# Kernel tuning notes

Hardware: AMD Instinct MI355X
Metric: run time of the kernel (lower is better)

The kernel has to match this reference:

```python
import jax, jax.numpy as jnp
import numpy as np

INF = 1e9  # large additive-mask constant (original code's INF)
D_KEY = 64


def setup_inputs() -> dict:
    key = jax.random.key(0)
    kq, kk, kv = jax.random.split(key, 3)
    B, S, D = 8, 2048, 64
    return {
        "query": jax.random.normal(kq, (B, S, D), dtype=jnp.float32),
        "key": jax.random.normal(kk, (B, S, D), dtype=jnp.float32),
        "value": jax.random.normal(kv, (B, S, D), dtype=jnp.float32),
    }


def reference(query, key, value):
    # scores: [B, Sq, Sk]
    scores = jnp.einsum("bqd,bkd->bqk", query, key)
    Sk = key.shape[1]
    # strict upper-triangular additive causal mask, subtracted BEFORE scaling
    tri = jnp.triu(jnp.ones((Sk, Sk), dtype=scores.dtype), k=1) * INF
    scores = scores - tri[None, :, :]
    scale = jnp.asarray(np.sqrt(D_KEY), dtype=scores.dtype)
    attn = jax.nn.softmax(scores / scale, axis=2)  # dropout ratio = 0.0
    return jnp.einsum("bqk,bkd->bqd", attn, value)
```

## Files before the change

### kernel.cpp

```cpp
#include <hip/hip_runtime.h>
#include <hip/hip_bf16.h>

typedef __attribute__((ext_vector_type(8))) short bf16x8;
typedef __attribute__((ext_vector_type(4))) float f32x4;
typedef __attribute__((ext_vector_type(4))) unsigned short us4;

#define BATCH 8
#define SEQ 2048
#define DIM 64
#define QB 64
#define NQT 32
#define NKT 32
#define TE 4096
#define CH 4
#define CPB 144
#define QSCALE (0.125f * 1.44269504088896f)
#define THR 8.0f

__device__ __forceinline__ unsigned short f2bf(float f) {
    return __builtin_bit_cast(unsigned short, __float2bfloat16(f));
}
__device__ __forceinline__ float bf2f(unsigned short u) {
    return __builtin_bit_cast(float, (unsigned)u << 16);
}

__device__ __forceinline__ int kswz(int row, int d) {
    return (row * DIM + d) ^ ((row & 7) << 3);
}
__device__ __forceinline__ int vswz(int d, int kv) {
    return (d * 64 + kv) ^ ((((d & 7) ^ ((d >> 2) & 7)) & 7) << 3);
}
__device__ __forceinline__ int pswz(int row, int kv) {
    return (row * 64 + kv) ^ ((row & 7) << 3);
}

#define GLOAD16(gsrc, ldst)                                                     \
    __builtin_amdgcn_global_load_lds(                                           \
        (const __attribute__((address_space(1))) void*)(gsrc),                  \
        (__attribute__((address_space(3))) void*)(ldst), 16, 0, 0)

__global__ __launch_bounds__(256) void prep_kernel(const float* __restrict__ K,
                                                   const float* __restrict__ V,
                                                   unsigned short* __restrict__ Kp,
                                                   unsigned short* __restrict__ Vp) {
    const int batch = blockIdx.x & 7;
    const int t = blockIdx.x >> 3;
    const int tile = batch * NKT + t;
    const int tid = threadIdx.x;
    const float* Kt = K + (size_t)tile * TE;
    const float* Vt = V + (size_t)tile * TE;
    unsigned short* Kd = Kp + (size_t)tile * TE;
    unsigned short* Vd = Vp + (size_t)tile * TE;
    #pragma unroll
    for (int i = 0; i < 4; ++i) {
        int idx = i * 256 + tid;
        int row = idx >> 4;
        int d0 = (idx & 15) << 2;
        f32x4 kf = *(const f32x4*)(Kt + row * DIM + d0);
        us4 kb = {f2bf(kf[0]), f2bf(kf[1]), f2bf(kf[2]), f2bf(kf[3])};
        *(us4*)(&Kd[kswz(row, d0)]) = kb;
    }
    const int dt4 = tid & 15, k4 = tid >> 4;
    f32x4 vf[4];
    #pragma unroll
    for (int rr = 0; rr < 4; ++rr)
        vf[rr] = *(const f32x4*)(Vt + (k4 * 4 + rr) * DIM + dt4 * 4);
    #pragma unroll
    for (int dd = 0; dd < 4; ++dd) {
        us4 vb = {f2bf(vf[0][dd]), f2bf(vf[1][dd]), f2bf(vf[2][dd]), f2bf(vf[3][dd])};
        *(us4*)(&Vd[vswz(dt4 * 4 + dd, k4 * 4)]) = vb;
    }
}

__global__ __launch_bounds__(256, 4) void fa_kernel(const float* __restrict__ Q,
                                                    const unsigned short* __restrict__ Kp,
                                                    const unsigned short* __restrict__ Vp,
                                                    unsigned short* __restrict__ PO,
                                                    float* __restrict__ PM,
                                                    float* __restrict__ PL,
                                                    float* __restrict__ O) {
    __shared__ unsigned short KL[2][4096];
    __shared__ unsigned short VL[2][4096];
    __shared__ unsigned short PB[4][1024];

    const int tid = threadIdx.x;
    const int w = tid >> 6, lane = tid & 63, g = lane >> 4, c = lane & 15;

    const int slot = blockIdx.x;
    const int batch = slot & 7;
    const int c0 = (CPB - 1) - (slot >> 3);
    int g2 = 0;
    #pragma unroll
    for (int gg = 1; gg < 8; ++gg) g2 = (c0 >= 2 * gg * (gg + 1)) ? gg : g2;
    const int nc = g2 + 1;
    const int x = c0 - 2 * g2 * nc;
    const int qrow = (x >= nc) + (x >= 2 * nc) + (x >= 3 * nc);
    const int sp = x - qrow * nc;
    const int qi = 4 * g2 + qrow;

    const int q0 = qi * QB;
    const int nt = qi + 1;
    const int t0 = sp * CH;
    const int t1 = (t0 + CH < nt) ? (t0 + CH) : nt;
    const int tiles = t1 - t0;
    const bool dchunk = (t1 == nt);

    const unsigned short* Kb = Kp + (size_t)batch * NKT * TE;
    const unsigned short* Vb = Vp + (size_t)batch * NKT * TE;

#define STAGE_TILE(tidx, buf)                                          \
    do {                                                               \
        const char* Ks_ = (const char*)(Kb + (size_t)(tidx) * TE);     \
        const char* Vs_ = (const char*)(Vb + (size_t)(tidx) * TE);     \
        char* kd_ = (char*)&KL[buf][0];                                \
        char* vd_ = (char*)&VL[buf][0];                                \
        _Pragma("unroll")                                              \
        for (int i_ = 0; i_ < 2; ++i_) {                               \
            int off_ = (w * 2 + i_) * 1024;                            \
            GLOAD16(Ks_ + off_ + lane * 16, kd_ + off_);               \
            GLOAD16(Vs_ + off_ + lane * 16, vd_ + off_);               \
        }                                                              \
    } while (0)

    STAGE_TILE(t0, 0);

    const float* Qrow = Q + (size_t)(batch * SEQ + q0 + w * 16 + c) * DIM;
    f32x4 qf0 = *(const f32x4*)(Qrow + g * 8);
    f32x4 qf1 = *(const f32x4*)(Qrow + g * 8 + 4);
    f32x4 qf2 = *(const f32x4*)(Qrow + 32 + g * 8);
    f32x4 qf3 = *(const f32x4*)(Qrow + 32 + g * 8 + 4);
    bf16x8 qa[2];
    #pragma unroll
    for (int j = 0; j < 4; ++j) {
        qa[0][j]     = (short)f2bf(qf0[j] * QSCALE);
        qa[0][j + 4] = (short)f2bf(qf1[j] * QSCALE);
        qa[1][j]     = (short)f2bf(qf2[j] * QSCALE);
        qa[1][j + 4] = (short)f2bf(qf3[j] * QSCALE);
    }

    float m[4], lsum[4];
    f32x4 o[4];
    #pragma unroll
    for (int r = 0; r < 4; ++r) { m[r] = -1e30f; lsum[r] = 0.f; }
    #pragma unroll
    for (int dt = 0; dt < 4; ++dt) o[dt] = f32x4{0.f, 0.f, 0.f, 0.f};

    __builtin_amdgcn_sched_barrier(0);
    asm volatile("s_waitcnt vmcnt(0)" ::: "memory");
    __builtin_amdgcn_s_barrier();
    __builtin_amdgcn_sched_barrier(0);

    for (int u = 0; u < tiles; ++u) {
        const int cb = u & 1;
        const bool last = (u == tiles - 1);

        if (!last) STAGE_TILE(t0 + u + 1, cb ^ 1);

        f32x4 s[4];
        #pragma unroll
        for (int n = 0; n < 4; ++n) s[n] = f32x4{0.f, 0.f, 0.f, 0.f};
        __builtin_amdgcn_s_setprio(1);
        #pragma unroll
        for (int n = 0; n < 4; ++n)
            #pragma unroll
            for (int f = 0; f < 2; ++f) {
                bf16x8 kb = *(bf16x8*)(&KL[cb][kswz(n * 16 + c, f * 32 + g * 8)]);
                s[n] = __builtin_amdgcn_mfma_f32_16x16x32_bf16(qa[f], kb, s[n], 0, 0, 0);
            }
        __builtin_amdgcn_s_setprio(0);

        if (dchunk && last) {
            const int dbase = (nt - 1) * 64;
            #pragma unroll
            for (int n = 0; n < 4; ++n) {
                int col = dbase + n * 16 + c;
                #pragma unroll
                for (int r = 0; r < 4; ++r)
                    if (col > q0 + w * 16 + g * 4 + r) s[n][r] = -1e30f;
            }
        }

        float pmx[4];
        #pragma unroll
        for (int r = 0; r < 4; ++r)
            pmx[r] = fmaxf(fmaxf(s[0][r], s[1][r]), fmaxf(s[2][r], s[3][r]));
        bool need = false;
        #pragma unroll
        for (int r = 0; r < 4; ++r) need |= (pmx[r] > m[r] + THR);
        if (__any(need)) {
            #pragma unroll
            for (int r = 0; r < 4; ++r) {
                float t2 = pmx[r];
                t2 = fmaxf(t2, __shfl_xor(t2, 1));
                t2 = fmaxf(t2, __shfl_xor(t2, 2));
                t2 = fmaxf(t2, __shfl_xor(t2, 4));
                t2 = fmaxf(t2, __shfl_xor(t2, 8));
                float mn = fmaxf(m[r], t2);
                float alpha = exp2f(m[r] - mn);
                m[r] = mn;
                lsum[r] *= alpha;
                #pragma unroll
                for (int dt = 0; dt < 4; ++dt) o[dt][r] *= alpha;
            }
        }
        #pragma unroll
        for (int n = 0; n < 4; ++n)
            #pragma unroll
            for (int r = 0; r < 4; ++r) {
                float pe = exp2f(s[n][r] - m[r]);
                s[n][r] = pe;
                lsum[r] += pe;
            }

        unsigned short* Pw = &PB[w][0];
        #pragma unroll
        for (int n = 0; n < 4; ++n)
            #pragma unroll
            for (int r = 0; r < 4; ++r)
                Pw[pswz(g * 4 + r, n * 16 + c)] = f2bf(s[n][r]);
        asm volatile("s_waitcnt lgkmcnt(0)" ::: "memory");
        __builtin_amdgcn_sched_barrier(0);

        __builtin_amdgcn_s_setprio(1);
        #pragma unroll
        for (int ks = 0; ks < 2; ++ks) {
            bf16x8 pa = *(bf16x8*)(&Pw[pswz(c, ks * 32 + g * 8)]);
            #pragma unroll
            for (int dt = 0; dt < 4; ++dt) {
                bf16x8 vb = *(bf16x8*)(&VL[cb][vswz(dt * 16 + c, ks * 32 + g * 8)]);
                o[dt] = __builtin_amdgcn_mfma_f32_16x16x32_bf16(pa, vb, o[dt], 0, 0, 0);
            }
        }
        __builtin_amdgcn_s_setprio(0);

        if (!last) {
            __builtin_amdgcn_sched_barrier(0);
            asm volatile("s_waitcnt vmcnt(0)" ::: "memory");
            __builtin_amdgcn_s_barrier();
            __builtin_amdgcn_sched_barrier(0);
        }
    }

    float l[4];
    #pragma unroll
    for (int r = 0; r < 4; ++r) {
        float ts = lsum[r];
        ts += __shfl_xor(ts, 1);
        ts += __shfl_xor(ts, 2);
        ts += __shfl_xor(ts, 4);
        ts += __shfl_xor(ts, 8);
        l[r] = ts;
    }

    if (nt <= CH) {
        #pragma unroll
        for (int r = 0; r < 4; ++r) {
            float inv = 1.f / l[r];
            float* Orow = O + (size_t)(batch * SEQ + q0 + w * 16 + g * 4 + r) * DIM;
            #pragma unroll
            for (int dt = 0; dt < 4; ++dt)
                Orow[dt * 16 + c] = o[dt][r] * inv;
        }
    } else {
        unsigned short* Pbase = PO + (size_t)slot * (QB * DIM);
        #pragma unroll
        for (int r = 0; r < 4; ++r) {
            int rowin = w * 16 + g * 4 + r;
            #pragma unroll
            for (int dt = 0; dt < 4; ++dt)
                Pbase[rowin * DIM + dt * 16 + c] = f2bf(o[dt][r]);
            if (c == 0) {
                PM[(size_t)slot * QB + rowin] = m[r];
                PL[(size_t)slot * QB + rowin] = l[r];
            }
        }
    }
#undef STAGE_TILE
}

__global__ __launch_bounds__(256) void combine_kernel(const unsigned short* __restrict__ PO,
                                                      const float* __restrict__ PM,
                                                      const float* __restrict__ PL,
                                                      float* __restrict__ O) {
    const int tid = threadIdx.x;
    const int ridx = blockIdx.x * 16 + (tid >> 4);
    const int d0 = (tid & 15) << 2;
    const int batch = ridx / 1792;
    const int rem = ridx - batch * 1792;
    const int qi = 4 + (rem >> 6);
    const int rowin = rem & 63;
    const int a = qi >> 2, b = qi & 3;
    const int nc = a + 1;
    const int pfx = (a + 1) * (2 * a + b);

    float mrun = -1e30f, ls = 0.f;
    f32x4 os = {0.f, 0.f, 0.f, 0.f};
    for (int sp = 0; sp < nc; ++sp) {
        int sl = ((CPB - 1 - (pfx + sp)) << 3) | batch;
        float mi = PM[(size_t)sl * QB + rowin];
        if (mi > mrun) {
            float sc = exp2f(mrun - mi);
            ls *= sc;
            os *= sc;
            mrun = mi;
        }
        float wgt = exp2f(mi - mrun);
        ls += PL[(size_t)sl * QB + rowin] * wgt;
        us4 po = *(const us4*)(PO + (size_t)sl * (QB * DIM) + rowin * DIM + d0);
        os[0] += bf2f(po[0]) * wgt;
        os[1] += bf2f(po[1]) * wgt;
        os[2] += bf2f(po[2]) * wgt;
        os[3] += bf2f(po[3]) * wgt;
    }
    const int grow = batch * SEQ + qi * 64 + rowin;
    float inv = 1.f / ls;
    f32x4 res = os * inv;
    *(f32x4*)(O + (size_t)grow * DIM + d0) = res;
}

extern "C" void kernel_launch(void* const* d_in, const int* in_sizes, int n_in,
                              void* d_out, int out_size, void* d_ws, size_t ws_size,
                              hipStream_t stream) {
    const float* Q = (const float*)d_in[0];
    const float* K = (const float*)d_in[1];
    const float* V = (const float*)d_in[2];
    float* O = (float*)d_out;
    (void)in_sizes; (void)n_in; (void)out_size; (void)ws_size;

    const size_t kvelems = (size_t)BATCH * SEQ * DIM;
    unsigned short* Kp = (unsigned short*)d_ws;
    unsigned short* Vp = Kp + kvelems;
    unsigned short* PO = Vp + kvelems;
    float* PM = (float*)(PO + (size_t)BATCH * CPB * QB * DIM);
    float* PL = PM + (size_t)BATCH * CPB * QB;

    prep_kernel<<<BATCH * NKT, 256, 0, stream>>>(K, V, Kp, Vp);
    fa_kernel<<<BATCH * CPB, 256, 0, stream>>>(Q, Kp, Vp, PO, PM, PL, O);
    combine_kernel<<<BATCH * 28 * 64 / 16, 256, 0, stream>>>(PO, PM, PL, O);
}
```

Baseline: 36.52 us.

## Compute transposed S so P stays in registers, dropping LDS round-trip for P

```diff
diff --git a/kernel.cpp b/kernel.cpp
--- a/kernel.cpp
+++ b/kernel.cpp
@@ -4,6 +4,7 @@
 typedef __attribute__((ext_vector_type(8))) short bf16x8;
 typedef __attribute__((ext_vector_type(4))) float f32x4;
 typedef __attribute__((ext_vector_type(4))) unsigned short us4;
+typedef __attribute__((ext_vector_type(4))) unsigned int u32x4;
 
 #define BATCH 8
 #define SEQ 2048
@@ -29,9 +30,6 @@
 }
 __device__ __forceinline__ int vswz(int d, int kv) {
     return (d * 64 + kv) ^ ((((d & 7) ^ ((d >> 2) & 7)) & 7) << 3);
-}
-__device__ __forceinline__ int pswz(int row, int kv) {
-    return (row * 64 + kv) ^ ((row & 7) << 3);
 }
 
 #define GLOAD16(gsrc, ldst)                                                     \
@@ -72,7 +70,7 @@
     }
 }
 
-__global__ __launch_bounds__(256, 4) void fa_kernel(const float* __restrict__ Q,
+__global__ __launch_bounds__(256, 5) void fa_kernel(const float* __restrict__ Q,
                                                     const unsigned short* __restrict__ Kp,
                                                     const unsigned short* __restrict__ Vp,
                                                     unsigned short* __restrict__ PO,
@@ -81,10 +79,10 @@
                                                     float* __restrict__ O) {
     __shared__ unsigned short KL[2][4096];
     __shared__ unsigned short VL[2][4096];
-    __shared__ unsigned short PB[4][1024];
 
     const int tid = threadIdx.x;
     const int w = tid >> 6, lane = tid & 63, g = lane >> 4, c = lane & 15;
+    const int gh = g >> 1;
 
     const int slot = blockIdx.x;
     const int batch = slot & 7;
@@ -138,10 +136,11 @@
         qa[1][j + 4] = (short)f2bf(qf3[j] * QSCALE);
     }
 
-    float m[4], lsum[4];
+    float mC = -1e30f, lsC = 0.f;
+    float mO[4];
     f32x4 o[4];
     #pragma unroll
-    for (int r = 0; r < 4; ++r) { m[r] = -1e30f; lsum[r] = 0.f; }
+    for (int r = 0; r < 4; ++r) mO[r] = -1e30f;
     #pragma unroll
     for (int dt = 0; dt < 4; ++dt) o[dt] = f32x4{0.f, 0.f, 0.f, 0.f};
 
@@ -165,66 +164,77 @@
             #pragma unroll
             for (int f = 0; f < 2; ++f) {
                 bf16x8 kb = *(bf16x8*)(&KL[cb][kswz(n * 16 + c, f * 32 + g * 8)]);
-                s[n] = __builtin_amdgcn_mfma_f32_16x16x32_bf16(qa[f], kb, s[n], 0, 0, 0);
+                s[n] = __builtin_amdgcn_mfma_f32_16x16x32_bf16(kb, qa[f], s[n], 0, 0, 0);
             }
         __builtin_amdgcn_s_setprio(0);
 
         if (dchunk && last) {
             const int dbase = (nt - 1) * 64;
-            #pragma unroll
-            for (int n = 0; n < 4; ++n) {
-                int col = dbase + n * 16 + c;
+            const int qg = q0 + w * 16 + c;
+            #pragma unroll
+            for (int n = 0; n < 4; ++n)
                 #pragma unroll
                 for (int r = 0; r < 4; ++r)
-                    if (col > q0 + w * 16 + g * 4 + r) s[n][r] = -1e30f;
-            }
-        }
-
-        float pmx[4];
-        #pragma unroll
-        for (int r = 0; r < 4; ++r)
-            pmx[r] = fmaxf(fmaxf(s[0][r], s[1][r]), fmaxf(s[2][r], s[3][r]));
-        bool need = false;
-        #pragma unroll
-        for (int r = 0; r < 4; ++r) need |= (pmx[r] > m[r] + THR);
-        if (__any(need)) {
+                    if (dbase + n * 16 + g * 4 + r > qg) s[n][r] = -1e30f;
+        }
+
+        float pmx = s[0][0];
+        #pragma unroll
+        for (int n = 0; n < 4; ++n)
+            #pragma unroll
+            for (int r = 0; r < 4; ++r) pmx = fmaxf(pmx, s[n][r]);
+        if (__any(pmx > mC + THR)) {
+            float t2 = pmx;
+            t2 = fmaxf(t2, __shfl_xor(t2, 16));
+            t2 = fmaxf(t2, __shfl_xor(t2, 32));
+            float mCn = fmaxf(mC, t2);
+            lsC *= exp2f(mC - mCn);
+            mC = mCn;
             #pragma unroll
             for (int r = 0; r < 4; ++r) {
-                float t2 = pmx[r];
-                t2 = fmaxf(t2, __shfl_xor(t2, 1));
-                t2 = fmaxf(t2, __shfl_xor(t2, 2));
-                t2 = fmaxf(t2, __shfl_xor(t2, 4));
-                t2 = fmaxf(t2, __shfl_xor(t2, 8));
-                float mn = fmaxf(m[r], t2);
-                float alpha = exp2f(m[r] - mn);
-                m[r] = mn;
-                lsum[r] *= alpha;
+                float mOn = __shfl(mCn, (lane & 48) | (g * 4 + r));
+                float al = exp2f(mO[r] - mOn);
+                mO[r] = mOn;
                 #pragma unroll
-                for (int dt = 0; dt < 4; ++dt) o[dt][r] *= alpha;
-            }
-        }
+                for (int dt = 0; dt < 4; ++dt) o[dt][r] *= al;
+            }
+        }
+        unsigned wpk[4][2];
         #pragma unroll
         for (int n = 0; n < 4; ++n)
             #pragma unroll
-            for (int r = 0; r < 4; ++r) {
-                float pe = exp2f(s[n][r] - m[r]);
-                s[n][r] = pe;
-                lsum[r] += pe;
-            }
-
-        unsigned short* Pw = &PB[w][0];
-        #pragma unroll
-        for (int n = 0; n < 4; ++n)
-            #pragma unroll
-            for (int r = 0; r < 4; ++r)
-                Pw[pswz(g * 4 + r, n * 16 + c)] = f2bf(s[n][r]);
-        asm volatile("s_waitcnt lgkmcnt(0)" ::: "memory");
-        __builtin_amdgcn_sched_barrier(0);
+            for (int rr = 0; rr < 2; ++rr) {
+                float pe0 = exp2f(s[n][2 * rr] - mC);
+                float pe1 = exp2f(s[n][2 * rr + 1] - mC);
+                lsC += pe0 + pe1;
+                wpk[n][rr] = ((unsigned)f2bf(pe1) << 16) | (unsigned)f2bf(pe0);
+            }
+
+        unsigned r1[2][2], r2[2][2];
+        #pragma unroll
+        for (int ks = 0; ks < 2; ++ks)
+            #pragma unroll
+            for (int rr = 0; rr < 2; ++rr)
+                r1[ks][rr] = (unsigned)__shfl_xor((int)wpk[(gh ^ 1) + 2 * ks][rr], 32);
+        const bool predR1 = (((g ^ gh) & 1) == 0);
+        #pragma unroll
+        for (int ks = 0; ks < 2; ++ks)
+            #pragma unroll
+            for (int rr = 0; rr < 2; ++rr) {
+                unsigned snd = predR1 ? r1[ks][rr] : wpk[gh + 2 * ks][rr];
+                r2[ks][rr] = (unsigned)__shfl_xor((int)snd, 16);
+            }
 
         __builtin_amdgcn_s_setprio(1);
         #pragma unroll
         for (int ks = 0; ks < 2; ++ks) {
-            bf16x8 pa = *(bf16x8*)(&Pw[pswz(c, ks * 32 + g * 8)]);
+            unsigned a0, a1, b0, b1;
+            if (g == 0)      { a0 = wpk[2*ks][0];   a1 = wpk[2*ks][1];   b0 = r2[ks][0]; b1 = r2[ks][1]; }
+            else if (g == 1) { a0 = r2[ks][0];      a1 = r2[ks][1];      b0 = r1[ks][0]; b1 = r1[ks][1]; }
+            else if (g == 2) { a0 = r1[ks][0];      a1 = r1[ks][1];      b0 = r2[ks][0]; b1 = r2[ks][1]; }
+            else             { a0 = r2[ks][0];      a1 = r2[ks][1];      b0 = wpk[1+2*ks][0]; b1 = wpk[1+2*ks][1]; }
+            u32x4 paw = {a0, a1, b0, b1};
+            bf16x8 pa = __builtin_bit_cast(bf16x8, paw);
             #pragma unroll
             for (int dt = 0; dt < 4; ++dt) {
                 bf16x8 vb = *(bf16x8*)(&VL[cb][vswz(dt * 16 + c, ks * 32 + g * 8)]);
@@ -241,21 +251,18 @@
         }
     }
 
-    float l[4];
-    #pragma unroll
-    for (int r = 0; r < 4; ++r) {
-        float ts = lsum[r];
-        ts += __shfl_xor(ts, 1);
-        ts += __shfl_xor(ts, 2);
-        ts += __shfl_xor(ts, 4);
-        ts += __shfl_xor(ts, 8);
-        l[r] = ts;
-    }
+    float lC = lsC;
+    lC += __shfl_xor(lC, 16);
+    lC += __shfl_xor(lC, 32);
+    float lO[4];
+    #pragma unroll
+    for (int r = 0; r < 4; ++r)
+        lO[r] = __shfl(lC, (lane & 48) | (g * 4 + r));
 
     if (nt <= CH) {
         #pragma unroll
         for (int r = 0; r < 4; ++r) {
-            float inv = 1.f / l[r];
+            float inv = 1.f / lO[r];
             float* Orow = O + (size_t)(batch * SEQ + q0 + w * 16 + g * 4 + r) * DIM;
             #pragma unroll
             for (int dt = 0; dt < 4; ++dt)
@@ -270,8 +277,8 @@
             for (int dt = 0; dt < 4; ++dt)
                 Pbase[rowin * DIM + dt * 16 + c] = f2bf(o[dt][r]);
             if (c == 0) {
-                PM[(size_t)slot * QB + rowin] = m[r];
-                PL[(size_t)slot * QB + rowin] = l[r];
+                PM[(size_t)slot * QB + rowin] = mO[r];
+                PL[(size_t)slot * QB + rowin] = lO[r];
             }
         }
     }
```

Measured after the change: 42.48 us. 16.3% more time.
